# Kernel tuning notes

Hardware: AMD Instinct MI355X
Metric: run time of the kernel (lower is better)

## Reference

```python
import jax, jax.numpy as jnp
import numpy as np

N_HEADS = 4
D_K = 64
SCALE = D_K ** -0.5


def setup_inputs() -> dict:
    key = jax.random.key(0)
    k1, k2, k3 = jax.random.split(key, 3)
    B, C, S = 8, 256, 2048
    x = jax.random.normal(k1, (B, C, S), dtype=jnp.float32)
    # Linear(C, 3*H*dk): weight [out, in] as in torch
    w_proj = jax.random.normal(k2, (3 * N_HEADS * D_K, C), dtype=jnp.float32) * (C ** -0.5)
    b_proj = jnp.zeros((3 * N_HEADS * D_K,), dtype=jnp.float32)
    w_out = jax.random.normal(k3, (C, N_HEADS * D_K), dtype=jnp.float32) * ((N_HEADS * D_K) ** -0.5)
    b_out = jnp.zeros((C,), dtype=jnp.float32)
    return {"x": x, "w_proj": w_proj, "b_proj": b_proj, "w_out": w_out, "b_out": b_out}


def reference(x, w_proj, b_proj, w_out, b_out):
    B, C, S = x.shape
    xt = jnp.transpose(x, (0, 2, 1))                    # [B, S, C]
    qkv = xt @ w_proj.T + b_proj                        # [B, S, 3*H*dk]
    qkv = qkv.reshape(B, S, N_HEADS, 3 * D_K)
    q, k, v = jnp.split(qkv, 3, axis=-1)                # each [B, S, H, dk]
    attn = jnp.einsum('bihd,bjhd->bijh', q, k) * SCALE  # [B, S, S, H]
    attn = jax.nn.softmax(attn, axis=2)                 # softmax over key axis j
    res = jnp.einsum('bijh,bjhd->bihd', attn, v)        # [B, S, H, dk]
    res = res.reshape(B, S, N_HEADS * D_K)
    res = res @ w_out.T + b_out + xt                    # residual in [B, S, C]
    return jnp.transpose(res, (0, 2, 1))                # back to [B, C, S]
```

## Files before the change

### kernel.cpp

```cpp
#include <hip/hip_runtime.h>


typedef _Float16 f16;
typedef __attribute__((ext_vector_type(4))) float f32x4;
typedef __attribute__((ext_vector_type(8))) _Float16 h8;
typedef __attribute__((ext_vector_type(4))) _Float16 h4;
typedef __attribute__((ext_vector_type(2))) __fp16 fp16x2;
typedef __attribute__((ext_vector_type(4))) __fp16 fp16x4;
typedef __attribute__((ext_vector_type(8))) __fp16 fp16x8;

#define SS 2048
#define CC 256
#define BB 8
#define HH 4
#define DK 64
#define O3 768
#define NT64 32
#define C1F 0.1803368801111204f
#define C2L2 11.541560327111707f

#define MFMA32(a, b, c) __builtin_amdgcn_mfma_f32_16x16x32_f16(a, b, c, 0, 0, 0)

#if __has_builtin(__builtin_amdgcn_exp2f)
#define EXP2(x) __builtin_amdgcn_exp2f(x)
#else
#define EXP2(x) exp2f(x)
#endif

__device__ __forceinline__ void async_ld16(const f16* g, f16* lds) {
  __builtin_amdgcn_global_load_lds(
      (const __attribute__((address_space(1))) unsigned int*)g,
      (__attribute__((address_space(3))) unsigned int*)lds, 16, 0, 0);
}

__global__ __launch_bounds__(256) void k_prep(const float* __restrict__ x,
                                              f16* __restrict__ xt,
                                              const float* __restrict__ w_proj,
                                              const float* __restrict__ w_out,
                                              f16* __restrict__ wp, f16* __restrict__ wo) {
  if (blockIdx.z == 8) {
    int slice = blockIdx.y * 32 + blockIdx.x;
    int i0 = slice * 2048 + threadIdx.x * 8;
    const float* src;
    f16* dst;
    if (i0 < O3 * CC) {
      src = w_proj + i0;
      int row = i0 >> 8, ch = (i0 & 255) >> 3;
      dst = wp + row * 256 + ((ch ^ (row & 7)) << 3);
    } else {
      int j = i0 - O3 * CC;
      src = w_out + j;
      int row = j >> 8, ch = (j & 255) >> 3;
      dst = wo + row * 256 + ((ch ^ (row & 7)) << 3);
    }
    float4 a = *(const float4*)src;
    float4 b = *(const float4*)(src + 4);
    h8 v = {(f16)a.x, (f16)a.y, (f16)a.z, (f16)a.w,
            (f16)b.x, (f16)b.y, (f16)b.z, (f16)b.w};
    *(h8*)dst = v;
    return;
  }
  __shared__ float tile[64][65];
  int b = blockIdx.z, c0 = blockIdx.y * 64, s0 = blockIdx.x * 64;
  int t = threadIdx.x;
#pragma unroll
  for (int it = 0; it < 16; ++it) {
    int idx = it * 256 + t;
    int cl = idx >> 6, sl = idx & 63;
    tile[cl][sl] = x[(size_t)(b * CC + c0 + cl) * SS + s0 + sl];
  }
  __syncthreads();
#pragma unroll
  for (int cid = t; cid < 512; cid += 256) {
    int sl = cid >> 3, chl = cid & 7;
    int s = s0 + sl;
    int gch = (c0 >> 3) + chl;
    h8 v;
#pragma unroll
    for (int e = 0; e < 8; ++e) v[e] = (f16)tile[chl * 8 + e][sl];
    *(h8*)(xt + (size_t)(b * SS + s) * CC + ((gch ^ (s & 7)) << 3)) = v;
  }
}

__global__ __launch_bounds__(256) void k_qkv(const f16* __restrict__ xt,
                                             const f16* __restrict__ wp,
                                             const float* __restrict__ bp,
                                             f16* __restrict__ qh, f16* __restrict__ ksw,
                                             f16* __restrict__ vsw) {
  __shared__ f16 As[16384];
  __shared__ f16 Bs[16384];
  __shared__ f16 Ot[4096];
  int b = blockIdx.z;
  int oti = blockIdx.y, o0 = oti * 64;
  int s0 = blockIdx.x * 64;
  int w = threadIdx.x >> 6, l = threadIdx.x & 63;
  int lr = l & 15, lg = l >> 4;

  const f16* Ag = xt + ((size_t)b * SS + s0) * CC;
  const f16* Bg = wp + (size_t)o0 * CC;
#pragma unroll
  for (int i = 0; i < 8; ++i) {
    int off = w * 4096 + i * 512;
    async_ld16(Ag + off + l * 8, &As[off]);
    async_ld16(Bg + off + l * 8, &Bs[off]);
  }
  asm volatile("s_waitcnt vmcnt(0)" ::: "memory");
  __syncthreads();

  f32x4 acc[4] = {};
#pragma unroll
  for (int kk = 0; kk < CC; kk += 32) {
    int chs = (((kk >> 3) + lg) ^ (lr & 7)) << 3;
    h8 af = *(const h8*)&As[(w * 16 + lr) * 256 + chs];
#pragma unroll
    for (int n = 0; n < 4; ++n) {
      h8 bf = *(const h8*)&Bs[(n * 16 + lr) * 256 + chs];
      acc[n] = MFMA32(af, bf, acc[n]);
    }
  }

  int seg = oti % 3;
  int h = oti / 3;
  int bh = b * HH + h;
  float scl = (seg == 0) ? C1F : 1.0f;
#pragma unroll
  for (int n = 0; n < 4; ++n) {
    float bb = bp[o0 + n * 16 + lr];
#pragma unroll
    for (int r = 0; r < 4; ++r) acc[n][r] = (acc[n][r] + bb) * scl;
  }

  if (seg == 2) {
#pragma unroll
    for (int n = 0; n < 4; ++n) {
      int d = n * 16 + lr;
#pragma unroll
      for (int r = 0; r < 4; ++r) {
        int sl = w * 16 + lg * 4 + r;
        int kl = sl & 31;
        int ps = ((kl & 15) >> 2) ^ ((d >> 1) & 3);
        Ot[(sl >> 5) * 2048 + d * 32 + ps * 8 + ((kl >> 4) << 2) + (kl & 3)] =
            (f16)acc[n][r];
      }
    }
  } else if (seg == 1) {
#pragma unroll
    for (int n = 0; n < 4; ++n) {
      int d = n * 16 + lr;
#pragma unroll
      for (int r = 0; r < 4; ++r) {
        int sl = w * 16 + lg * 4 + r;
        int kl = sl & 31;
        Ot[(sl >> 5) * 2048 + kl * 64 + (((d >> 3) ^ (kl & 7)) << 3) + (d & 7)] =
            (f16)acc[n][r];
      }
    }
  } else {
#pragma unroll
    for (int n = 0; n < 4; ++n)
#pragma unroll
      for (int r = 0; r < 4; ++r)
        Ot[(w * 16 + lg * 4 + r) * 64 + n * 16 + lr] = (f16)acc[n][r];
  }
  __syncthreads();

  int t = threadIdx.x;
  f16* dst;
  if (seg == 0)
    dst = qh + ((size_t)bh * SS + s0) * DK;
  else if (seg == 1)
    dst = ksw + ((size_t)bh * NT64 + (s0 >> 6)) * 4096;
  else
    dst = vsw + ((size_t)bh * NT64 + (s0 >> 6)) * 4096;
  *(int4*)(dst + t * 16) = *(const int4*)&Ot[t * 16];
  *(int4*)(dst + t * 16 + 8) = *(const int4*)&Ot[t * 16 + 8];
}

__global__ __launch_bounds__(256) void k_attn(const f16* __restrict__ qh,
                                              const f16* __restrict__ ksw,
                                              const f16* __restrict__ vsw,
                                              f16* __restrict__ res) {
  __shared__ f16 kbuf[2][4096];
  __shared__ f16 vbuf[2][4096];
  int id = blockIdx.x;
  int xcd = id & 7, slot = id >> 3;
  int bh = xcd * 4 + (slot >> 5);
  int qt = slot & 31;
  int w = threadIdx.x >> 6, l = threadIdx.x & 63;
  int q0 = qt * 64 + w * 16;
  int lr = l & 15, lg = l >> 4;

  const f16* qp = qh + (size_t)(bh * SS + q0 + lr) * DK;
  h8 qf0 = *(const h8*)(qp + lg * 8);
  h8 qf1 = *(const h8*)(qp + 32 + lg * 8);

  const f16* kg = ksw + (size_t)bh * (SS * DK);
  const f16* vg = vsw + (size_t)bh * (SS * DK);

#define STAGE(bufi, tile)                                           \
  {                                                                 \
    const f16* kq = kg + (size_t)(tile) * 4096 + w * 1024 + l * 8;  \
    const f16* vq = vg + (size_t)(tile) * 4096 + w * 1024 + l * 8;  \
    f16* kd = &kbuf[bufi][w * 1024];                                \
    f16* vd = &vbuf[bufi][w * 1024];                                \
    async_ld16(kq, kd);                                             \
    async_ld16(kq + 512, kd + 512);                                 \
    async_ld16(vq, vd);                                             \
    async_ld16(vq + 512, vd + 512);                                 \
  }

  int swk = (lr & 7) << 3;
  int ek[2][2];
#pragma unroll
  for (int kb = 0; kb < 2; ++kb)
#pragma unroll
    for (int ch = 0; ch < 2; ++ch)
      ek[kb][ch] = (lr + kb * 16) * 64 + ((ch * 32 + lg * 8) ^ swk);
  int ev = lr * 32 + ((lg ^ ((lr >> 1) & 3)) * 8);

  f32x4 oacc[4] = {};
  f32x4 dacc = {};
  const f32x4 cinit = {-C2L2, -C2L2, -C2L2, -C2L2};
  const h8 ones8 = {(f16)1.0f, (f16)1.0f, (f16)1.0f, (f16)1.0f,
                    (f16)1.0f, (f16)1.0f, (f16)1.0f, (f16)1.0f};

  STAGE(0, 0);
  STAGE(1, 1);

  for (int kt = 0; kt < NT64; ++kt) {
    int cur = kt & 1;
    asm volatile("s_waitcnt vmcnt(4)" ::: "memory");
    __builtin_amdgcn_sched_barrier(0);
    __builtin_amdgcn_s_barrier();
    __builtin_amdgcn_sched_barrier(0);

    const f16* kb_ = kbuf[cur];
    const f16* vb_ = vbuf[cur];
#pragma unroll
    for (int sub = 0; sub < 2; ++sub) {
      int sb = sub * 2048;
      h8 kf[2][2];
#pragma unroll
      for (int kb = 0; kb < 2; ++kb)
#pragma unroll
        for (int ch = 0; ch < 2; ++ch) kf[kb][ch] = *(const h8*)&kb_[sb + ek[kb][ch]];
      h8 vv[4];
#pragma unroll
      for (int m = 0; m < 4; ++m) vv[m] = *(const h8*)&vb_[sb + ev + m * 512];

      __builtin_amdgcn_s_setprio(1);
      f32x4 sacc[2];
#pragma unroll
      for (int kb = 0; kb < 2; ++kb) {
        sacc[kb] = MFMA32(kf[kb][0], qf0, cinit);
        sacc[kb] = MFMA32(kf[kb][1], qf1, sacc[kb]);
      }
      float e0 = EXP2(sacc[0][0]);
      float e1 = EXP2(sacc[0][1]);
      float e2 = EXP2(sacc[0][2]);
      float e3 = EXP2(sacc[0][3]);
      float e4 = EXP2(sacc[1][0]);
      float e5 = EXP2(sacc[1][1]);
      float e6 = EXP2(sacc[1][2]);
      float e7 = EXP2(sacc[1][3]);
      fp16x2 p01 = __builtin_amdgcn_cvt_pkrtz(e0, e1);
      fp16x2 p23 = __builtin_amdgcn_cvt_pkrtz(e2, e3);
      fp16x2 p45 = __builtin_amdgcn_cvt_pkrtz(e4, e5);
      fp16x2 p67 = __builtin_amdgcn_cvt_pkrtz(e6, e7);
      fp16x4 lo4 = __builtin_shufflevector(p01, p23, 0, 1, 2, 3);
      fp16x4 hi4 = __builtin_shufflevector(p45, p67, 0, 1, 2, 3);
      fp16x8 p8 = __builtin_shufflevector(lo4, hi4, 0, 1, 2, 3, 4, 5, 6, 7);
      h8 pf8 = __builtin_bit_cast(h8, p8);

      dacc = MFMA32(ones8, pf8, dacc);
#pragma unroll
      for (int m = 0; m < 4; ++m) oacc[m] = MFMA32(vv[m], pf8, oacc[m]);
      __builtin_amdgcn_s_setprio(0);
    }

    __builtin_amdgcn_sched_barrier(0);
    __builtin_amdgcn_s_barrier();
    __builtin_amdgcn_sched_barrier(0);
    int nxt = (kt + 2) & (NT64 - 1);
    STAGE(cur, nxt);
  }

  int b = bh >> 2, h = bh & 3;
  float inv = 1.0f / dacc[0];
  int s = q0 + lr;
  f16* rrow = res + (size_t)(b * SS + s) * CC;
  int sk = s & 7;
#pragma unroll
  for (int m = 0; m < 4; ++m) {
    int d = h * 64 + m * 16 + lg * 4;
    int ch = d >> 3;
    h4 rv;
#pragma unroll
    for (int r = 0; r < 4; ++r) rv[r] = (f16)(oacc[m][r] * inv);
    *(h4*)(rrow + ((ch ^ sk) << 3) + (d & 7)) = rv;
  }
}

__global__ __launch_bounds__(256) void k_out(const f16* __restrict__ res,
                                             const f16* __restrict__ wo,
                                             const float* __restrict__ bo,
                                             const float* __restrict__ x,
                                             float* __restrict__ out) {
  __shared__ f16 As[16384];
  __shared__ f16 Bs[16384];
  __shared__ float Xs[4096];
  float* Ot = (float*)As;

  int b = blockIdx.z;
  int c0 = blockIdx.y * 64;
  int s0 = blockIdx.x * 64;
  int w = threadIdx.x >> 6, l = threadIdx.x & 63;
  int lr = l & 15, lg = l >> 4;

  const f16* Ag = res + ((size_t)b * SS + s0) * CC;
  const f16* Bg = wo + (size_t)c0 * CC;
#pragma unroll
  for (int i = 0; i < 8; ++i) {
    int off = w * 4096 + i * 512;
    async_ld16(Ag + off + l * 8, &As[off]);
    async_ld16(Bg + off + l * 8, &Bs[off]);
  }
#pragma unroll
  for (int i = 0; i < 4; ++i) {
    int cl = w * 16 + i * 4 + (l >> 4);
    int cidx = l & 15;
    const float* src =
        x + ((size_t)b * CC + c0 + cl) * SS + s0 + ((cidx ^ (cl & 7)) << 2);
    async_ld16((const f16*)src, (f16*)&Xs[w * 1024 + i * 256 + l * 4]);
  }
  asm volatile("s_waitcnt vmcnt(0)" ::: "memory");
  __syncthreads();

  f32x4 acc[4] = {};
#pragma unroll
  for (int kk = 0; kk < CC; kk += 32) {
    int chs = (((kk >> 3) + lg) ^ (lr & 7)) << 3;
    h8 af = *(const h8*)&As[(w * 16 + lr) * 256 + chs];
#pragma unroll
    for (int n = 0; n < 4; ++n) {
      h8 bf = *(const h8*)&Bs[(n * 16 + lr) * 256 + chs];
      acc[n] = MFMA32(af, bf, acc[n]);
    }
  }
  __syncthreads();

#pragma unroll
  for (int n = 0; n < 4; ++n) {
    int c = c0 + n * 16 + lr;
    float bb = bo[c];
    float4 xv =
        *(const float4*)&Xs[(n * 16 + lr) * 64 + (((w * 4 + lg) ^ (lr & 7)) << 2)];
    float4 ov;
    ov.x = acc[n][0] + bb + xv.x;
    ov.y = acc[n][1] + bb + xv.y;
    ov.z = acc[n][2] + bb + xv.z;
    ov.w = acc[n][3] + bb + xv.w;
    *(float4*)&Ot[(n * 16 + lr) * 68 + w * 16 + lg * 4] = ov;
  }
  __syncthreads();

  int cl = threadIdx.x >> 2, sc = (threadIdx.x & 3) * 16;
  float* orow = out + ((size_t)b * CC + c0 + cl) * SS + s0 + sc;
  const float* srow = &Ot[cl * 68 + sc];
#pragma unroll
  for (int j = 0; j < 4; ++j) *(float4*)(orow + j * 4) = *(const float4*)(srow + j * 4);
}

extern "C" void kernel_launch(void* const* d_in, const int* in_sizes, int n_in,
                              void* d_out, int out_size, void* d_ws, size_t ws_size,
                              hipStream_t stream) {
  const float* x = (const float*)d_in[0];
  const float* w_proj = (const float*)d_in[1];
  const float* b_proj = (const float*)d_in[2];
  const float* w_out = (const float*)d_in[3];
  const float* b_out = (const float*)d_in[4];
  float* out = (float*)d_out;

  char* p = (char*)d_ws;
  f16* xt = (f16*)p; p += (size_t)BB * SS * CC * 2;
  f16* wp = (f16*)p; p += (size_t)O3 * CC * 2;
  f16* wo = (f16*)p; p += (size_t)CC * CC * 2;
  f16* qh = (f16*)p; p += (size_t)BB * HH * SS * DK * 2;
  f16* ksw = (f16*)p; p += (size_t)BB * HH * SS * DK * 2;
  f16* vsw = (f16*)p; p += (size_t)BB * HH * SS * DK * 2;
  f16* res = (f16*)p;

  k_prep<<<dim3(SS / 64, CC / 64, BB + 1), 256, 0, stream>>>(x, xt, w_proj, w_out, wp, wo);
  k_qkv<<<dim3(SS / 64, O3 / 64, BB), 256, 0, stream>>>(xt, wp, b_proj, qh, ksw, vsw);
  k_attn<<<dim3(1024), 256, 0, stream>>>(qh, ksw, vsw, res);
  k_out<<<dim3(SS / 64, CC / 64, BB), 256, 0, stream>>>(res, wo, b_out, x, out);
}
```

Baseline: 91.98 us.

## Split attention waves across query and key halves with LDS reduction

Each wave now handles 32 query rows and one half of every 64-key tile, instead of 16 query rows over the whole tile. Each K/V fragment read from LDS is therefore reused for two query sub-tiles, which roughly halves LDS reads per MFMA. The two key-half partial outputs and denominators are combined through LDS at the end of the kernel. In exchange it uses more accumulator registers, adds an extra reduction barrier and epilogue, and sets a min-blocks occupancy hint of 4 on the launch bounds.

```diff
diff --git a/kernel.cpp b/kernel.cpp
--- a/kernel.cpp
+++ b/kernel.cpp
@@ -176,10 +176,10 @@
   *(int4*)(dst + t * 16 + 8) = *(const int4*)&Ot[t * 16 + 8];
 }
 
-__global__ __launch_bounds__(256) void k_attn(const f16* __restrict__ qh,
-                                              const f16* __restrict__ ksw,
-                                              const f16* __restrict__ vsw,
-                                              f16* __restrict__ res) {
+__global__ __launch_bounds__(256, 4) void k_attn(const f16* __restrict__ qh,
+                                                 const f16* __restrict__ ksw,
+                                                 const f16* __restrict__ vsw,
+                                                 f16* __restrict__ res) {
   __shared__ f16 kbuf[2][4096];
   __shared__ f16 vbuf[2][4096];
   int id = blockIdx.x;
@@ -187,26 +187,31 @@
   int bh = xcd * 4 + (slot >> 5);
   int qt = slot & 31;
   int w = threadIdx.x >> 6, l = threadIdx.x & 63;
-  int q0 = qt * 64 + w * 16;
+  int qg = w & 1, kg = w >> 1;
+  int q0w = qt * 64 + qg * 32;
   int lr = l & 15, lg = l >> 4;
 
-  const f16* qp = qh + (size_t)(bh * SS + q0 + lr) * DK;
-  h8 qf0 = *(const h8*)(qp + lg * 8);
-  h8 qf1 = *(const h8*)(qp + 32 + lg * 8);
-
-  const f16* kg = ksw + (size_t)bh * (SS * DK);
-  const f16* vg = vsw + (size_t)bh * (SS * DK);
-
-#define STAGE(bufi, tile)                                           \
-  {                                                                 \
-    const f16* kq = kg + (size_t)(tile) * 4096 + w * 1024 + l * 8;  \
-    const f16* vq = vg + (size_t)(tile) * 4096 + w * 1024 + l * 8;  \
-    f16* kd = &kbuf[bufi][w * 1024];                                \
-    f16* vd = &vbuf[bufi][w * 1024];                                \
-    async_ld16(kq, kd);                                             \
-    async_ld16(kq + 512, kd + 512);                                 \
-    async_ld16(vq, vd);                                             \
-    async_ld16(vq + 512, vd + 512);                                 \
+  h8 qf[2][2];
+#pragma unroll
+  for (int qs = 0; qs < 2; ++qs) {
+    const f16* qp = qh + (size_t)(bh * SS + q0w + qs * 16 + lr) * DK;
+    qf[qs][0] = *(const h8*)(qp + lg * 8);
+    qf[qs][1] = *(const h8*)(qp + 32 + lg * 8);
+  }
+
+  const f16* kg_ = ksw + (size_t)bh * (SS * DK);
+  const f16* vg_ = vsw + (size_t)bh * (SS * DK);
+
+#define STAGE(bufi, tile)                                            \
+  {                                                                  \
+    const f16* kq = kg_ + (size_t)(tile) * 4096 + w * 1024 + l * 8;  \
+    const f16* vq = vg_ + (size_t)(tile) * 4096 + w * 1024 + l * 8;  \
+    f16* kd = &kbuf[bufi][w * 1024];                                 \
+    f16* vd = &vbuf[bufi][w * 1024];                                 \
+    async_ld16(kq, kd);                                              \
+    async_ld16(kq + 512, kd + 512);                                  \
+    async_ld16(vq, vd);                                              \
+    async_ld16(vq + 512, vd + 512);                                  \
   }
 
   int swk = (lr & 7) << 3;
@@ -218,11 +223,13 @@
       ek[kb][ch] = (lr + kb * 16) * 64 + ((ch * 32 + lg * 8) ^ swk);
   int ev = lr * 32 + ((lg ^ ((lr >> 1) & 3)) * 8);
 
-  f32x4 oacc[4] = {};
-  f32x4 dacc = {};
+  f32x4 oacc[2][4] = {};
+  f32x4 dacc[2] = {};
   const f32x4 cinit = {-C2L2, -C2L2, -C2L2, -C2L2};
   const h8 ones8 = {(f16)1.0f, (f16)1.0f, (f16)1.0f, (f16)1.0f,
                     (f16)1.0f, (f16)1.0f, (f16)1.0f, (f16)1.0f};
+
+  int sb = kg * 2048;
 
   STAGE(0, 0);
   STAGE(1, 1);
@@ -234,35 +241,37 @@
     __builtin_amdgcn_s_barrier();
     __builtin_amdgcn_sched_barrier(0);
 
-    const f16* kb_ = kbuf[cur];
-    const f16* vb_ = vbuf[cur];
-#pragma unroll
-    for (int sub = 0; sub < 2; ++sub) {
-      int sb = sub * 2048;
-      h8 kf[2][2];
-#pragma unroll
-      for (int kb = 0; kb < 2; ++kb)
-#pragma unroll
-        for (int ch = 0; ch < 2; ++ch) kf[kb][ch] = *(const h8*)&kb_[sb + ek[kb][ch]];
-      h8 vv[4];
-#pragma unroll
-      for (int m = 0; m < 4; ++m) vv[m] = *(const h8*)&vb_[sb + ev + m * 512];
-
-      __builtin_amdgcn_s_setprio(1);
-      f32x4 sacc[2];
+    const f16* kb_ = &kbuf[cur][sb];
+    const f16* vb_ = &vbuf[cur][sb];
+    h8 kf[2][2];
+#pragma unroll
+    for (int kb = 0; kb < 2; ++kb)
+#pragma unroll
+      for (int ch = 0; ch < 2; ++ch) kf[kb][ch] = *(const h8*)&kb_[ek[kb][ch]];
+    h8 vv[4];
+#pragma unroll
+    for (int m = 0; m < 4; ++m) vv[m] = *(const h8*)&vb_[ev + m * 512];
+
+    __builtin_amdgcn_s_setprio(1);
+    f32x4 sacc[2][2];
+#pragma unroll
+    for (int qs = 0; qs < 2; ++qs)
 #pragma unroll
       for (int kb = 0; kb < 2; ++kb) {
-        sacc[kb] = MFMA32(kf[kb][0], qf0, cinit);
-        sacc[kb] = MFMA32(kf[kb][1], qf1, sacc[kb]);
+        sacc[qs][kb] = MFMA32(kf[kb][0], qf[qs][0], cinit);
+        sacc[qs][kb] = MFMA32(kf[kb][1], qf[qs][1], sacc[qs][kb]);
       }
-      float e0 = EXP2(sacc[0][0]);
-      float e1 = EXP2(sacc[0][1]);
-      float e2 = EXP2(sacc[0][2]);
-      float e3 = EXP2(sacc[0][3]);
-      float e4 = EXP2(sacc[1][0]);
-      float e5 = EXP2(sacc[1][1]);
-      float e6 = EXP2(sacc[1][2]);
-      float e7 = EXP2(sacc[1][3]);
+    h8 pf8[2];
+#pragma unroll
+    for (int qs = 0; qs < 2; ++qs) {
+      float e0 = EXP2(sacc[qs][0][0]);
+      float e1 = EXP2(sacc[qs][0][1]);
+      float e2 = EXP2(sacc[qs][0][2]);
+      float e3 = EXP2(sacc[qs][0][3]);
+      float e4 = EXP2(sacc[qs][1][0]);
+      float e5 = EXP2(sacc[qs][1][1]);
+      float e6 = EXP2(sacc[qs][1][2]);
+      float e7 = EXP2(sacc[qs][1][3]);
       fp16x2 p01 = __builtin_amdgcn_cvt_pkrtz(e0, e1);
       fp16x2 p23 = __builtin_amdgcn_cvt_pkrtz(e2, e3);
       fp16x2 p45 = __builtin_amdgcn_cvt_pkrtz(e4, e5);
@@ -270,13 +279,15 @@
       fp16x4 lo4 = __builtin_shufflevector(p01, p23, 0, 1, 2, 3);
       fp16x4 hi4 = __builtin_shufflevector(p45, p67, 0, 1, 2, 3);
       fp16x8 p8 = __builtin_shufflevector(lo4, hi4, 0, 1, 2, 3, 4, 5, 6, 7);
-      h8 pf8 = __builtin_bit_cast(h8, p8);
-
-      dacc = MFMA32(ones8, pf8, dacc);
-#pragma unroll
-      for (int m = 0; m < 4; ++m) oacc[m] = MFMA32(vv[m], pf8, oacc[m]);
-      __builtin_amdgcn_s_setprio(0);
-    }
+      pf8[qs] = __builtin_bit_cast(h8, p8);
+    }
+#pragma unroll
+    for (int qs = 0; qs < 2; ++qs) dacc[qs] = MFMA32(ones8, pf8[qs], dacc[qs]);
+#pragma unroll
+    for (int qs = 0; qs < 2; ++qs)
+#pragma unroll
+      for (int m = 0; m < 4; ++m) oacc[qs][m] = MFMA32(vv[m], pf8[qs], oacc[qs][m]);
+    __builtin_amdgcn_s_setprio(0);
 
     __builtin_amdgcn_sched_barrier(0);
     __builtin_amdgcn_s_barrier();
@@ -285,19 +296,40 @@
     STAGE(cur, nxt);
   }
 
-  int b = bh >> 2, h = bh & 3;
-  float inv = 1.0f / dacc[0];
-  int s = q0 + lr;
-  f16* rrow = res + (size_t)(b * SS + s) * CC;
-  int sk = s & 7;
-#pragma unroll
-  for (int m = 0; m < 4; ++m) {
-    int d = h * 64 + m * 16 + lg * 4;
-    int ch = d >> 3;
-    h4 rv;
-#pragma unroll
-    for (int r = 0; r < 4; ++r) rv[r] = (f16)(oacc[m][r] * inv);
-    *(h4*)(rrow + ((ch ^ sk) << 3) + (d & 7)) = rv;
+  asm volatile("s_waitcnt vmcnt(0)" ::: "memory");
+  __syncthreads();
+
+  float* red = (float*)&kbuf[0][0];
+  float* redd = (float*)&vbuf[0][0];
+  if (kg == 1) {
+#pragma unroll
+    for (int qs = 0; qs < 2; ++qs) {
+#pragma unroll
+      for (int m = 0; m < 4; ++m)
+        *(f32x4*)&red[(qg * 8 + qs * 4 + m) * 256 + l * 4] = oacc[qs][m];
+      redd[(qg * 2 + qs) * 64 + l] = dacc[qs][0];
+    }
+  }
+  __syncthreads();
+  if (kg == 0) {
+    int b = bh >> 2, h = bh & 3;
+#pragma unroll
+    for (int qs = 0; qs < 2; ++qs) {
+      float inv = 1.0f / (dacc[qs][0] + redd[(qg * 2 + qs) * 64 + l]);
+      int s = q0w + qs * 16 + lr;
+      f16* rrow = res + (size_t)(b * SS + s) * CC;
+      int sk = s & 7;
+#pragma unroll
+      for (int m = 0; m < 4; ++m) {
+        f32x4 o2 = *(const f32x4*)&red[(qg * 8 + qs * 4 + m) * 256 + l * 4];
+        int d = h * 64 + m * 16 + lg * 4;
+        int ch = d >> 3;
+        h4 rv;
+#pragma unroll
+        for (int r = 0; r < 4; ++r) rv[r] = (f16)((oacc[qs][m][r] + o2[r]) * inv);
+        *(h4*)(rrow + ((ch ^ sk) << 3) + (d & 7)) = rv;
+      }
+    }
   }
 }
 
```

Result: faster. 85.87 us, median of 3 (-6.6%).
